# Optimization experiments

Hardware: AMD Instinct MI355X
Metric: run time of the kernel (lower is better)

Reference implementation:

```python
import jax, jax.numpy as jnp
import numpy as np


def setup_inputs() -> dict:
    key = jax.random.key(0)
    ks = jax.random.split(key, 7)
    B, F, D = 1024, 32, 64
    H = [128, 128, 128]
    x = jax.random.normal(ks[0], (B, F, D), dtype=jnp.float32)
    # Conv1d(k=1) weights: (out, in) where in = prev_field * F, Kaiming-ish scale
    W0 = jax.random.normal(ks[1], (H[0], F * F), dtype=jnp.float32) * 0.02
    b0 = jnp.zeros((H[0],), dtype=jnp.float32)
    W1 = jax.random.normal(ks[2], (H[1], H[0] * F), dtype=jnp.float32) * 0.02
    b1 = jnp.zeros((H[1],), dtype=jnp.float32)
    W2 = jax.random.normal(ks[3], (H[2], H[1] * F), dtype=jnp.float32) * 0.02
    b2 = jnp.zeros((H[2],), dtype=jnp.float32)
    return {"x": x, "W0": W0, "b0": b0, "W1": W1, "b1": b1, "W2": W2, "b2": b2}


def reference(x, W0, b0, W1, b1, W2, b2):
    # CIN: per layer, outer product of current hidden with base fields along
    # embed dim, then 1x1 conv (channel mix) + ReLU. We fuse the bhmd
    # intermediate directly into the contraction: W reshaped to (o, h, m)
    # matches torch's reshape(b, h*m, d) channel ordering (h major, m minor).
    F = x.shape[1]
    x0 = x  # (b, m=F, d)
    h = x
    res = []
    for W, b in ((W0, b0), (W1, b1), (W2, b2)):
        o = W.shape[0]
        Wr = W.reshape(o, h.shape[1], F)  # (o, h, m)
        z = jnp.einsum('bhd,bmd,ohm->bod', h, x0, Wr) + b[None, :, None]
        h = jax.nn.relu(z)
        res.append(h)
    out = jnp.concatenate(res, axis=1)  # (b, sum(H), d)
    return jnp.sum(out, axis=-1)  # (b, sum(H))
```

## Files before the change

### kernel.cpp

```cpp
#include <hip/hip_runtime.h>
#include <stdint.h>


typedef __attribute__((ext_vector_type(8))) _Float16 f16x8;
typedef __attribute__((ext_vector_type(2))) _Float16 f16x2;
typedef __attribute__((ext_vector_type(4))) float f32x4;
typedef __attribute__((ext_vector_type(4))) int i32x4;

union AB {
  i32x4 i;
  f16x8 h;
  uint32_t u[4];
};

static __device__ __forceinline__ uint32_t pkmul(uint32_t a, uint32_t b) {
  f16x2 r = __builtin_bit_cast(f16x2, a) * __builtin_bit_cast(f16x2, b);
  return __builtin_bit_cast(uint32_t, r);
}
static __device__ __forceinline__ uint32_t pkcvt(float a, float b) {
  return __builtin_bit_cast(uint32_t, __builtin_amdgcn_cvt_pkrtz(a, b));
}

#define HP 136

__global__ __launch_bounds__(512, 4) void cin_main(
    const float* __restrict__ x, const uint16_t* __restrict__ wp,
    const float* __restrict__ bias0, const float* __restrict__ bias1,
    const float* __restrict__ bias2, float* __restrict__ out) {
  __shared__ __align__(16) uint16_t hT[2][64][HP];

  const int tid = threadIdx.x;
  const int w = tid >> 6, lane = tid & 63;
  const int p = w >> 2;
  const int wg = w & 3;
  const int q = lane >> 4;
  const int i = lane & 15;
  const int bb = blockIdx.x * 2;

  for (int e = tid; e < 4096; e += 512) {
    int p2 = e >> 11, m = (e >> 6) & 31, d = e & 63;
    hT[p2][d][m] =
        __builtin_bit_cast(uint16_t, (_Float16)x[(size_t)(bb + p2) * 2048 + m * 64 + d]);
  }
  __syncthreads();

  AB xf[4];
#pragma unroll
  for (int t = 0; t < 4; ++t)
    xf[t].i = *(const i32x4*)&hT[p][t * 16 + i][q * 8];

  f32x4 acc[4][2];

#pragma unroll
  for (int L = 0; L < 3; ++L) {
    const int Kch = (L == 0) ? 32 : 128;
    const uint16_t* wl = (L == 0) ? wp : (L == 1) ? wp + 131072 : wp + 655360;
    const float* bias = (L == 0) ? bias0 : (L == 1) ? bias1 : bias2;

    const uint16_t* wptr0 = wl + (size_t)(2 * wg + 0) * Kch * 512 + lane * 8;
    const uint16_t* wptr1 = wl + (size_t)(2 * wg + 1) * Kch * 512 + lane * 8;

#pragma unroll
    for (int t = 0; t < 4; ++t)
#pragma unroll
      for (int g = 0; g < 2; ++g) acc[t][g] = (f32x4){0.f, 0.f, 0.f, 0.f};

    AB wbuf[2][2][2];
    uint32_t hvA[4], hvB[4];

    auto loadSlot = [&](int s, int c) {
      int cw = (c < Kch) ? c : 0;
#pragma unroll
      for (int cc = 0; cc < 2; ++cc) {
        wbuf[s][cc][0].i = *(const i32x4*)(wptr0 + (size_t)(cw + cc) * 512);
        wbuf[s][cc][1].i = *(const i32x4*)(wptr1 + (size_t)(cw + cc) * 512);
      }
    };
    auto loadHv = [&](uint32_t (&hv)[4], int c) {
      int cw = (c < Kch) ? c : 0;
#pragma unroll
      for (int t = 0; t < 4; ++t)
        hv[t] = *(const uint32_t*)&hT[p][t * 16 + i][cw];
    };
    auto computePair = [&](const AB (&wb)[2][2], const uint32_t (&hv)[4]) {
#pragma unroll
      for (int cc = 0; cc < 2; ++cc)
#pragma unroll
        for (int t = 0; t < 4; ++t) {
          uint32_t hd = __builtin_amdgcn_perm(hv[t], hv[t],
                                              cc ? 0x03020302u : 0x01000100u);
          AB bf;
#pragma unroll
          for (int k = 0; k < 4; ++k) bf.u[k] = pkmul(hd, xf[t].u[k]);
          acc[t][0] = __builtin_amdgcn_mfma_f32_16x16x32_f16(wb[cc][0].h, bf.h, acc[t][0], 0, 0, 0);
          acc[t][1] = __builtin_amdgcn_mfma_f32_16x16x32_f16(wb[cc][1].h, bf.h, acc[t][1], 0, 0, 0);
        }
    };

    loadSlot(0, 0);
    loadSlot(1, 2);
    loadHv(hvA, 0);

#pragma unroll 1
    for (int c0 = 0; c0 < Kch; c0 += 4) {
      loadHv(hvB, c0 + 2);
      computePair(wbuf[0], hvA);
      loadSlot(0, c0 + 4);
      __builtin_amdgcn_sched_barrier(0);
      loadHv(hvA, c0 + 4);
      computePair(wbuf[1], hvB);
      loadSlot(1, c0 + 6);
      __builtin_amdgcn_sched_barrier(0);
    }

    f32x4 bv[2];
    bv[0] = *(const f32x4*)(bias + (2 * wg + 0) * 16 + q * 4);
    bv[1] = *(const f32x4*)(bias + (2 * wg + 1) * 16 + q * 4);
#pragma unroll
    for (int t = 0; t < 4; ++t)
#pragma unroll
      for (int g = 0; g < 2; ++g)
#pragma unroll
        for (int r = 0; r < 4; ++r)
          acc[t][g][r] = fmaxf(acc[t][g][r] + bv[g][r], 0.f);

    if (L < 2) {
      __syncthreads();
#pragma unroll
      for (int t = 0; t < 4; ++t)
#pragma unroll
        for (int g = 0; g < 2; ++g) {
          uint2 pk;
          pk.x = pkcvt(acc[t][g][0], acc[t][g][1]);
          pk.y = pkcvt(acc[t][g][2], acc[t][g][3]);
          *(uint2*)&hT[p][t * 16 + i][(2 * wg + g) * 16 + q * 4] = pk;
        }
    }

#pragma unroll
    for (int g = 0; g < 2; ++g)
#pragma unroll
      for (int r = 0; r < 4; ++r) {
        float s = acc[0][g][r] + acc[1][g][r] + acc[2][g][r] + acc[3][g][r];
        s += __shfl_xor(s, 1);
        s += __shfl_xor(s, 2);
        s += __shfl_xor(s, 4);
        s += __shfl_xor(s, 8);
        if (i == 0)
          out[(size_t)(bb + p) * 384 + L * 128 + (2 * wg + g) * 16 + q * 4 + r] = s;
      }

    if (L < 2) __syncthreads();
  }
}

__global__ void pack_w_all(const float* __restrict__ W0, const float* __restrict__ W1,
                           const float* __restrict__ W2, uint16_t* __restrict__ Wp) {
  int blk = blockIdx.x;
  const float* W;
  uint16_t* dst;
  int kshift;
  if (blk < 64)       { W = W0; dst = Wp;          kshift = 5; }
  else if (blk < 320) { W = W1; dst = Wp + 131072; kshift = 7; blk -= 64; }
  else                { W = W2; dst = Wp + 655360; kshift = 7; blk -= 320; }
  int idx = blk * 256 + threadIdx.x;
  int Kq = 1 << (kshift + 2);
  int o = idx >> (kshift + 2);
  int kq = idx & (Kq - 1);
  int c = kq >> 2, q = kq & 3;
  int ot = o >> 4, ii = o & 15;
  const float* src = W + ((size_t)o << (kshift + 5)) + kq * 8;
  uint4 val;
  val.x = pkcvt(src[0], src[1]);
  val.y = pkcvt(src[2], src[3]);
  val.z = pkcvt(src[4], src[5]);
  val.w = pkcvt(src[6], src[7]);
  *(uint4*)(dst + ((((size_t)ot << kshift) + c) << 9) + (q << 7) + (ii << 3)) = val;
}

extern "C" void kernel_launch(void* const* d_in, const int* in_sizes, int n_in,
                              void* d_out, int out_size, void* d_ws, size_t ws_size,
                              hipStream_t stream) {
  (void)in_sizes; (void)n_in; (void)out_size; (void)ws_size;
  const float* x  = (const float*)d_in[0];
  const float* W0 = (const float*)d_in[1];
  const float* b0 = (const float*)d_in[2];
  const float* W1 = (const float*)d_in[3];
  const float* b1 = (const float*)d_in[4];
  const float* W2 = (const float*)d_in[5];
  const float* b2 = (const float*)d_in[6];
  uint16_t* wpacked = (uint16_t*)d_ws;

  hipLaunchKernelGGL(pack_w_all, dim3(576), dim3(256), 0, stream, W0, W1, W2, wpacked);
  hipLaunchKernelGGL(cin_main, dim3(512), dim3(512), 0, stream,
                     x, wpacked, b0, b1, b2, (float*)d_out);
}
```

Baseline: 199.5 us.

## Assign one batch per block with each wave owning one output tile

Each block now handles one batch element instead of two, and each of the 8 waves computes a single 16-output tile instead of two. The grid doubles to 1024 blocks, shared memory per block halves, and launch bounds rise to 6 blocks per CU to raise occupancy. In exchange, each weight fragment loaded from global memory now feeds one MFMA instead of two, so weight traffic per unit of work roughly doubles and the outer-product pkmul work is no longer shared across two output groups.

Measured after the change: 233.0 us. 16.8% more time.

```diff
diff --git a/kernel.cpp b/kernel.cpp
--- a/kernel.cpp
+++ b/kernel.cpp
@@ -23,33 +23,31 @@
 
 #define HP 136
 
-__global__ __launch_bounds__(512, 4) void cin_main(
+__global__ __launch_bounds__(512, 6) void cin_main(
     const float* __restrict__ x, const uint16_t* __restrict__ wp,
     const float* __restrict__ bias0, const float* __restrict__ bias1,
     const float* __restrict__ bias2, float* __restrict__ out) {
-  __shared__ __align__(16) uint16_t hT[2][64][HP];
+  __shared__ __align__(16) uint16_t hT[64][HP];
 
   const int tid = threadIdx.x;
   const int w = tid >> 6, lane = tid & 63;
-  const int p = w >> 2;
-  const int wg = w & 3;
   const int q = lane >> 4;
   const int i = lane & 15;
-  const int bb = blockIdx.x * 2;
+  const int b = blockIdx.x;
 
-  for (int e = tid; e < 4096; e += 512) {
-    int p2 = e >> 11, m = (e >> 6) & 31, d = e & 63;
-    hT[p2][d][m] =
-        __builtin_bit_cast(uint16_t, (_Float16)x[(size_t)(bb + p2) * 2048 + m * 64 + d]);
+  for (int e = tid; e < 2048; e += 512) {
+    int m = e >> 6, d = e & 63;
+    hT[d][m] =
+        __builtin_bit_cast(uint16_t, (_Float16)x[(size_t)b * 2048 + m * 64 + d]);
   }
   __syncthreads();
 
   AB xf[4];
 #pragma unroll
   for (int t = 0; t < 4; ++t)
-    xf[t].i = *(const i32x4*)&hT[p][t * 16 + i][q * 8];
+    xf[t].i = *(const i32x4*)&hT[t * 16 + i][q * 8];
 
-  f32x4 acc[4][2];
+  f32x4 acc[4];
 
 #pragma unroll
   for (int L = 0; L < 3; ++L) {
@@ -57,32 +55,27 @@
     const uint16_t* wl = (L == 0) ? wp : (L == 1) ? wp + 131072 : wp + 655360;
     const float* bias = (L == 0) ? bias0 : (L == 1) ? bias1 : bias2;
 
-    const uint16_t* wptr0 = wl + (size_t)(2 * wg + 0) * Kch * 512 + lane * 8;
-    const uint16_t* wptr1 = wl + (size_t)(2 * wg + 1) * Kch * 512 + lane * 8;
+    const uint16_t* wptr = wl + (size_t)w * Kch * 512 + lane * 8;
 
 #pragma unroll
-    for (int t = 0; t < 4; ++t)
-#pragma unroll
-      for (int g = 0; g < 2; ++g) acc[t][g] = (f32x4){0.f, 0.f, 0.f, 0.f};
+    for (int t = 0; t < 4; ++t) acc[t] = (f32x4){0.f, 0.f, 0.f, 0.f};
 
-    AB wbuf[2][2][2];
+    AB wbuf[2][2];
     uint32_t hvA[4], hvB[4];
 
     auto loadSlot = [&](int s, int c) {
       int cw = (c < Kch) ? c : 0;
 #pragma unroll
-      for (int cc = 0; cc < 2; ++cc) {
-        wbuf[s][cc][0].i = *(const i32x4*)(wptr0 + (size_t)(cw + cc) * 512);
-        wbuf[s][cc][1].i = *(const i32x4*)(wptr1 + (size_t)(cw + cc) * 512);
-      }
+      for (int cc = 0; cc < 2; ++cc)
+        wbuf[s][cc].i = *(const i32x4*)(wptr + (size_t)(cw + cc) * 512);
     };
     auto loadHv = [&](uint32_t (&hv)[4], int c) {
       int cw = (c < Kch) ? c : 0;
 #pragma unroll
       for (int t = 0; t < 4; ++t)
-        hv[t] = *(const uint32_t*)&hT[p][t * 16 + i][cw];
+        hv[t] = *(const uint32_t*)&hT[t * 16 + i][cw];
     };
-    auto computePair = [&](const AB (&wb)[2][2], const uint32_t (&hv)[4]) {
+    auto computePair = [&](const AB (&wb)[2], const uint32_t (&hv)[4]) {
 #pragma unroll
       for (int cc = 0; cc < 2; ++cc)
 #pragma unroll
@@ -92,8 +85,8 @@
           AB bf;
 #pragma unroll
           for (int k = 0; k < 4; ++k) bf.u[k] = pkmul(hd, xf[t].u[k]);
-          acc[t][0] = __builtin_amdgcn_mfma_f32_16x16x32_f16(wb[cc][0].h, bf.h, acc[t][0], 0, 0, 0);
-          acc[t][1] = __builtin_amdgcn_mfma_f32_16x16x32_f16(wb[cc][1].h, bf.h, acc[t][1], 0, 0, 0);
+          acc[t] = __builtin_amdgcn_mfma_f32_16x16x32_f16(wb[cc].h, bf.h,
+                                                          acc[t], 0, 0, 0);
         }
     };
 
@@ -113,42 +106,34 @@
       __builtin_amdgcn_sched_barrier(0);
     }
 
-    f32x4 bv[2];
-    bv[0] = *(const f32x4*)(bias + (2 * wg + 0) * 16 + q * 4);
-    bv[1] = *(const f32x4*)(bias + (2 * wg + 1) * 16 + q * 4);
+    f32x4 bv = *(const f32x4*)(bias + w * 16 + q * 4);
 #pragma unroll
     for (int t = 0; t < 4; ++t)
 #pragma unroll
-      for (int g = 0; g < 2; ++g)
-#pragma unroll
-        for (int r = 0; r < 4; ++r)
-          acc[t][g][r] = fmaxf(acc[t][g][r] + bv[g][r], 0.f);
+      for (int r = 0; r < 4; ++r)
+        acc[t][r] = fmaxf(acc[t][r] + bv[r], 0.f);
 
     if (L < 2) {
       __syncthreads();
 #pragma unroll
-      for (int t = 0; t < 4; ++t)
-#pragma unroll
-        for (int g = 0; g < 2; ++g) {
-          uint2 pk;
-          pk.x = pkcvt(acc[t][g][0], acc[t][g][1]);
-          pk.y = pkcvt(acc[t][g][2], acc[t][g][3]);
-          *(uint2*)&hT[p][t * 16 + i][(2 * wg + g) * 16 + q * 4] = pk;
-        }
+      for (int t = 0; t < 4; ++t) {
+        uint2 pk;
+        pk.x = pkcvt(acc[t][0], acc[t][1]);
+        pk.y = pkcvt(acc[t][2], acc[t][3]);
+        *(uint2*)&hT[t * 16 + i][w * 16 + q * 4] = pk;
+      }
     }
 
 #pragma unroll
-    for (int g = 0; g < 2; ++g)
-#pragma unroll
-      for (int r = 0; r < 4; ++r) {
-        float s = acc[0][g][r] + acc[1][g][r] + acc[2][g][r] + acc[3][g][r];
-        s += __shfl_xor(s, 1);
-        s += __shfl_xor(s, 2);
-        s += __shfl_xor(s, 4);
-        s += __shfl_xor(s, 8);
-        if (i == 0)
-          out[(size_t)(bb + p) * 384 + L * 128 + (2 * wg + g) * 16 + q * 4 + r] = s;
-      }
+    for (int r = 0; r < 4; ++r) {
+      float s = acc[0][r] + acc[1][r] + acc[2][r] + acc[3][r];
+      s += __shfl_xor(s, 1);
+      s += __shfl_xor(s, 2);
+      s += __shfl_xor(s, 4);
+      s += __shfl_xor(s, 8);
+      if (i == 0)
+        out[(size_t)b * 384 + L * 128 + w * 16 + q * 4 + r] = s;
+    }
 
     if (L < 2) __syncthreads();
   }
@@ -192,6 +177,6 @@
   uint16_t* wpacked = (uint16_t*)d_ws;
 
   hipLaunchKernelGGL(pack_w_all, dim3(576), dim3(256), 0, stream, W0, W1, W2, wpacked);
-  hipLaunchKernelGGL(cin_main, dim3(512), dim3(512), 0, stream,
+  hipLaunchKernelGGL(cin_main, dim3(1024), dim3(512), 0, stream,
                      x, wpacked, b0, b1, b2, (float*)d_out);
 }
```
